# Performance work log

Measured on AMD Instinct MI355X. Metric: run time of the kernel, lower is better.

Reference implementation:

```python
import jax, jax.numpy as jnp
import numpy as np

WS = 8          # window_size
NH = 8          # num_heads
DIM = 512
EPS = 1e-5


def _layernorm(x, gamma, beta):
    mu = jnp.mean(x, axis=-1, keepdims=True)
    var = jnp.mean(jnp.square(x - mu), axis=-1, keepdims=True)
    return (x - mu) * jax.lax.rsqrt(var + EPS) * gamma + beta


def setup_inputs() -> dict:
    key = jax.random.key(0)
    ks = jax.random.split(key, 16)
    B, C, H, W = 8, DIM, 128, 128
    s = 0.02
    return {
        "x": jax.random.normal(ks[0], (B, C, H, W), jnp.float32),
        "gamma1": jnp.ones((C,), jnp.float32),
        "beta1": jnp.zeros((C,), jnp.float32),
        "gamma2": jnp.ones((C,), jnp.float32),
        "beta2": jnp.zeros((C,), jnp.float32),
        "w_qkv": jax.random.normal(ks[1], (C, 3 * C), jnp.float32) * s,
        "b_qkv": jnp.zeros((3 * C,), jnp.float32),
        "w_out": jax.random.normal(ks[2], (C, C), jnp.float32) * s,
        "b_out": jnp.zeros((C,), jnp.float32),
        "w1": jax.random.normal(ks[3], (C, 4 * C), jnp.float32) * s,
        "b1": jnp.zeros((4 * C,), jnp.float32),
        "w2": jax.random.normal(ks[4], (4 * C, C), jnp.float32) * s,
        "b2": jnp.zeros((C,), jnp.float32),
    }


def reference(x, gamma1, beta1, gamma2, beta2, w_qkv, b_qkv, w_out, b_out, w1, b1, w2, b2):
    B, C, H, W = x.shape
    hd = C // NH          # head_dim = 64
    L = WS * WS           # tokens per window = 64
    N = (H // WS) * (W // WS)

    # window_partition: (B,C,H,W) -> (B,N,C,ws,ws)
    xw = x.reshape(B, C, H // WS, WS, W // WS, WS)
    xw = xw.transpose(0, 1, 2, 4, 3, 5).reshape(B, C, N, WS, WS).transpose(0, 2, 1, 3, 4)
    # spatial_flatten -> (B,N,L,C)
    t = xw.reshape(B, N, C, L).transpose(0, 1, 3, 2)

    # --- attention (non-transposed path) ---
    xn = _layernorm(t, gamma1, beta1)
    qkv = jnp.einsum('bnlc,cd->bnld', xn, w_qkv) + b_qkv
    qkv = qkv.reshape(B, N, L, 3, NH, hd).transpose(3, 0, 1, 4, 2, 5)  # (3,B,N,H,L,hd)
    q, k, v = qkv[0], qkv[1], qkv[2]
    # note: module scales by 1/head_dim on BOTH q and k -> 1/hd^2 total
    scores = jnp.einsum('bnhld,bnhmd->bnhlm', q, k) / (hd * hd)
    attn = jax.nn.softmax(scores, axis=-1)
    o = jnp.einsum('bnhlm,bnhmd->bnhld', attn, v)
    o = o.transpose(0, 1, 3, 2, 4).reshape(B, N, L, C)
    o = jnp.einsum('bnlc,cd->bnld', o, w_out) + b_out
    t = t + o

    # --- MLP ---
    xn2 = _layernorm(t, gamma2, beta2)
    h = jax.nn.gelu(jnp.einsum('bnlc,cd->bnld', xn2, w1) + b1, approximate=False)
    t = t + jnp.einsum('bnld,dc->bnlc', h, w2) + b2

    # spatial_unflatten + window_unpartition -> (B,C,H,W)
    y = t.transpose(0, 1, 3, 2).reshape(B, N, C, WS, WS).transpose(0, 2, 1, 3, 4)
    y = y.reshape(B, C, H // WS, W // WS, WS, WS).transpose(0, 1, 2, 4, 3, 5).reshape(B, C, H, W)
    return y
```

## Files before the change

### kernel.cpp

```cpp
#include <hip/hip_runtime.h>
#include <cstdint>
#include <cstddef>


typedef unsigned short u16;
typedef unsigned int u32;
typedef __attribute__((ext_vector_type(4))) float f32x4;
typedef __attribute__((ext_vector_type(8))) short bf16x8;

#define DEVINL __device__ __forceinline__

DEVINL float bf2f(u16 u){ union { u32 i; float f; } v; v.i = ((u32)u) << 16; return v.f; }
DEVINL u16 f2bf(float f){
  union { float f; u32 i; } v; v.f = f;
  u32 u = v.i;
  u32 r = (u + 0x7fffu + ((u >> 16) & 1u)) >> 16;
  return (u16)r;
}

DEVINL void gload16(u16* lds, const void* g){
  __builtin_amdgcn_global_load_lds(
      (__attribute__((address_space(1))) u32*)(g),
      (__attribute__((address_space(3))) u32*)(lds), 16, 0, 0);
}

__global__ __launch_bounds__(256) void wt_kernel(const float* __restrict__ in,
                                                 u16* __restrict__ out, int K, int N)
{
  __shared__ float tile[64][65];
  int tiles_n = N >> 6;
  int tk = blockIdx.x / tiles_n, tn = blockIdx.x % tiles_n;
  int k0 = tk * 64, n0 = tn * 64;
  int lane = threadIdx.x & 63, wr = threadIdx.x >> 6;
#pragma unroll
  for (int i = 0; i < 16; i++){
    int r = wr * 16 + i;
    tile[r][lane] = in[(size_t)(k0 + r) * N + n0 + lane];
  }
  __syncthreads();
#pragma unroll
  for (int i = 0; i < 16; i++){
    int r = wr * 16 + i;
    out[(size_t)(n0 + r) * K + k0 + lane] = f2bf(tile[lane][r]);
  }
}

template<int MODE>
__global__ __launch_bounds__(256) void ln_kernel(
    const float* __restrict__ x, const u16* __restrict__ o2,
    const float* __restrict__ gamma, const float* __restrict__ beta,
    u16* __restrict__ out)
{
  __shared__ u16 sm[512 * 64];
  int wg = blockIdx.x;
  int b = wg >> 8, n = wg & 255, wy = n >> 4, wx = n & 15;
  int t = threadIdx.x, l = t & 63, wv = t >> 6;
  int yy = l >> 3, xx = l & 7;
  size_t xbase = ((size_t)b * 512) * 16384 + (size_t)(wy * 8 + yy) * 128 + wx * 8 + xx;

#pragma unroll 4
  for (int i = 0; i < 128; i++){
    int c = wv * 128 + i;
    float v = x[xbase + (size_t)c * 16384];
    sm[c * 64 + (l ^ ((2 * (c >> 3)) & 63))] = f2bf(v);
  }
  __syncthreads();

  size_t gbase = (size_t)wg * 64;
  int lane = l;
  int c0 = lane * 8;
  int fs = (2 * lane) & 63;
  float g8[8], b8[8];
#pragma unroll
  for (int j = 0; j < 8; j++){ g8[j] = gamma[c0 + j]; b8[j] = beta[c0 + j]; }

  for (int it = 0; it < 16; it++){
    int tok = wv * 16 + it;
    int lidx = tok ^ fs;
    u16 oarr[8];
    if (MODE == 1){
      uint4 ov = *(const uint4*)&o2[(gbase + tok) * 512 + c0];
      *(uint4*)oarr = ov;
    }
    float tv[8]; float sum = 0.f, sq = 0.f;
#pragma unroll
    for (int j = 0; j < 8; j++){
      float v = bf2f(sm[(c0 + j) * 64 + lidx]);
      if (MODE == 1) v += bf2f(oarr[j]);
      tv[j] = v; sum += v; sq += v * v;
    }
#pragma unroll
    for (int d = 1; d < 64; d <<= 1){
      sum += __shfl_xor(sum, d, 64);
      sq  += __shfl_xor(sq, d, 64);
    }
    float mu = sum * (1.0f / 512.0f);
    float var = sq * (1.0f / 512.0f) - mu * mu;
    float rs = rsqrtf(var + 1e-5f);
    u16 r8[8];
#pragma unroll
    for (int j = 0; j < 8; j++) r8[j] = f2bf((tv[j] - mu) * rs * g8[j] + b8[j]);
    *(uint4*)&out[(gbase + tok) * 512 + c0] = *(uint4*)r8;
  }
}

template<int EPI>
__global__ __launch_bounds__(512, 2) void gemm256_kernel(
    const u16* __restrict__ A, const u16* __restrict__ BT,
    const float* __restrict__ bias, const u16* __restrict__ ADD,
    u16* __restrict__ Cout, int N, int K)
{
  __shared__ u16 smem[65536];
  const int nbn = N >> 8;
  int nwg = gridDim.x;
  int bid = blockIdx.x;
  int wgid = (bid & 7) * (nwg >> 3) + (bid >> 3);
  int bm = wgid / nbn, bn = wgid % nbn;
  size_t m0 = (size_t)bm * 256; int n0 = bn * 256;
  int tid = threadIdx.x;
  int lane = tid & 63, w = tid >> 6;
  int wr = w >> 2, wc = w & 3;

  f32x4 zero4 = {0.f, 0.f, 0.f, 0.f};
  f32x4 acc[8][4];
#pragma unroll
  for (int i = 0; i < 8; i++)
#pragma unroll
    for (int j = 0; j < 4; j++) acc[i][j] = zero4;

  int sr = tid >> 2;
  int scol = (((tid & 3) ^ ((sr >> 1) & 3)) * 8);
  const u16* Abase = A + m0 * (size_t)K;
  const u16* Bbase = BT + (size_t)n0 * K;

  auto STAGE = [&](int slot, int kt){
    u16* s = &smem[slot * 16384];
    gload16(s + w * 512,          Abase + (size_t)sr * K + kt + scol);
    gload16(s + 4096 + w * 512,   Abase + (size_t)(sr + 128) * K + kt + scol);
    gload16(s + 8192 + w * 512,   Bbase + (size_t)sr * K + kt + scol);
    gload16(s + 12288 + w * 512,  Bbase + (size_t)(sr + 128) * K + kt + scol);
  };

  int nk = K >> 5;
  STAGE(0, 0); STAGE(1, 32); STAGE(2, 64);

  int kslot = lane >> 4;
  for (int t = 0; t < nk; ++t){
    if (t < nk - 2)      asm volatile("s_waitcnt vmcnt(8)" ::: "memory");
    else if (t == nk - 2) asm volatile("s_waitcnt vmcnt(4)" ::: "memory");
    else                  asm volatile("s_waitcnt vmcnt(0)" ::: "memory");
    __builtin_amdgcn_s_barrier();
    if (t + 3 < nk) STAGE((t + 3) & 3, (t + 3) << 5);

    const u16* as = &smem[(t & 3) * 16384];
    const u16* bs = as + 8192;
    bf16x8 af[8], bf[4];
#pragma unroll
    for (int m = 0; m < 8; m++){
      int row = wr * 128 + m * 16 + (lane & 15);
      af[m] = *(const bf16x8*)&as[row * 32 + ((kslot ^ ((row >> 1) & 3)) * 8)];
    }
#pragma unroll
    for (int n = 0; n < 4; n++){
      int row = wc * 64 + n * 16 + (lane & 15);
      bf[n] = *(const bf16x8*)&bs[row * 32 + ((kslot ^ ((row >> 1) & 3)) * 8)];
    }
    __builtin_amdgcn_s_setprio(1);
#pragma unroll
    for (int m = 0; m < 8; m++)
#pragma unroll
      for (int n = 0; n < 4; n++)
        acc[m][n] = __builtin_amdgcn_mfma_f32_16x16x32_bf16(af[m], bf[n], acc[m][n], 0, 0, 0);
    __builtin_amdgcn_s_setprio(0);
  }

  __syncthreads();

#pragma unroll
  for (int n = 0; n < 4; n++){
    int cc = wc * 64 + n * 16 + (lane & 15);
    float bv = bias[n0 + cc];
#pragma unroll
    for (int m = 0; m < 8; m++){
      int r0 = wr * 128 + m * 16 + ((lane >> 4) * 4);
#pragma unroll
      for (int reg = 0; reg < 4; reg++){
        int rr = r0 + reg;
        float v = acc[m][n][reg] + bv;
        if (EPI == 1){
          float h2 = v * v;
          float z = -1.5957691216057308f * (v + 0.044715f * v * h2);
          float e = __expf(z);
          v = v * __builtin_amdgcn_rcpf(1.0f + e);
        }
        smem[rr * 256 + (cc ^ ((rr & 31) << 3))] = f2bf(v);
      }
    }
  }
  __syncthreads();

#pragma unroll
  for (int i = 0; i < 16; i++){
    int c = i * 512 + tid;
    int row = c >> 5, g = c & 31;
    size_t gro = (m0 + row) * (size_t)N + n0 + g * 8;
    uint4 d = *(const uint4*)&smem[row * 256 + ((g ^ (row & 31)) << 3)];
    if (EPI == 2){
      uint4 av = *(const uint4*)&ADD[gro];
      u16 de[8], ae[8];
      *(uint4*)de = d; *(uint4*)ae = av;
#pragma unroll
      for (int k = 0; k < 8; k++) de[k] = f2bf(bf2f(de[k]) + bf2f(ae[k]));
      d = *(uint4*)de;
    }
    *(uint4*)&Cout[gro] = d;
  }
}

__global__ __launch_bounds__(64) void attn_kernel(const u16* __restrict__ QKV,
                                                  u16* __restrict__ O)
{
  __shared__ u16 qs[4096], ks2[4096], vs[4096], ps[4096];
  int blk = blockIdx.x;
  int wg = blk >> 3, h = blk & 7;
  size_t g0 = (size_t)wg * 64;
  int lane = threadIdx.x;
  int lr = lane >> 3, lch = lane & 7;

#pragma unroll
  for (int it = 0; it < 8; it++){
    int r = it * 8 + lr;
    int sc = lch ^ (r & 7);
    {
      uint4 d = *(const uint4*)&QKV[(g0 + r) * 1536 + h * 64 + lch * 8];
      *(uint4*)&qs[r * 64 + sc * 8] = d;
    }
    {
      uint4 d = *(const uint4*)&QKV[(g0 + r) * 1536 + 512 + h * 64 + lch * 8];
      *(uint4*)&ks2[r * 64 + sc * 8] = d;
    }
    {
      uint4 d = *(const uint4*)&QKV[(g0 + r) * 1536 + 1024 + h * 64 + lch * 8];
      u16 e[8]; *(uint4*)e = d;
      int m = r;
#pragma unroll
      for (int j = 0; j < 8; j++){
        int dd = lch * 8 + j;
        int off = dd * 64 + ((((m * 2) ^ ((dd & 7) << 4))) >> 1);
        vs[off] = e[j];
      }
    }
  }
  __syncthreads();

  f32x4 zero4 = {0.f, 0.f, 0.f, 0.f};
  f32x4 s[4][4];
#pragma unroll
  for (int i = 0; i < 4; i++)
#pragma unroll
    for (int j = 0; j < 4; j++) s[i][j] = zero4;

#pragma unroll
  for (int ks = 0; ks < 2; ks++){
    bf16x8 aq[4], bk[4];
#pragma unroll
    for (int mt = 0; mt < 4; mt++){
      int r = mt * 16 + (lane & 15);
      int cb = (ks * 64 + (lane >> 4) * 16) ^ ((r & 7) << 4);
      aq[mt] = *(const bf16x8*)&qs[r * 64 + (cb >> 1)];
    }
#pragma unroll
    for (int nt = 0; nt < 4; nt++){
      int r = nt * 16 + (lane & 15);
      int cb = (ks * 64 + (lane >> 4) * 16) ^ ((r & 7) << 4);
      bk[nt] = *(const bf16x8*)&ks2[r * 64 + (cb >> 1)];
    }
#pragma unroll
    for (int mt = 0; mt < 4; mt++)
#pragma unroll
      for (int nt = 0; nt < 4; nt++)
        s[mt][nt] = __builtin_amdgcn_mfma_f32_16x16x32_bf16(aq[mt], bk[nt], s[mt][nt], 0, 0, 0);
  }

  const float scl = 1.0f / 4096.0f;
#pragma unroll
  for (int mt = 0; mt < 4; mt++){
#pragma unroll
    for (int reg = 0; reg < 4; reg++){
      float mx = -1e30f;
#pragma unroll
      for (int nt = 0; nt < 4; nt++){
        float v = s[mt][nt][reg] * scl; s[mt][nt][reg] = v; mx = fmaxf(mx, v);
      }
#pragma unroll
      for (int d = 1; d < 16; d <<= 1) mx = fmaxf(mx, __shfl_xor(mx, d, 64));
      float sum = 0.f;
#pragma unroll
      for (int nt = 0; nt < 4; nt++){
        float e = __expf(s[mt][nt][reg] - mx); s[mt][nt][reg] = e; sum += e;
      }
#pragma unroll
      for (int d = 1; d < 16; d <<= 1) sum += __shfl_xor(sum, d, 64);
      float inv = 1.0f / sum;
#pragma unroll
      for (int nt = 0; nt < 4; nt++) s[mt][nt][reg] *= inv;
    }
  }

#pragma unroll
  for (int mt = 0; mt < 4; mt++)
#pragma unroll
    for (int reg = 0; reg < 4; reg++){
      int r = mt * 16 + ((lane >> 4) * 4) + reg;
#pragma unroll
      for (int nt = 0; nt < 4; nt++){
        int c = nt * 16 + (lane & 15);
        ps[r * 64 + ((((c * 2) ^ ((r & 7) << 4))) >> 1)] = f2bf(s[mt][nt][reg]);
      }
    }
  __syncthreads();

  f32x4 o[4][4];
#pragma unroll
  for (int i = 0; i < 4; i++)
#pragma unroll
    for (int j = 0; j < 4; j++) o[i][j] = zero4;

#pragma unroll
  for (int ks = 0; ks < 2; ks++){
    bf16x8 ap[4], bv[4];
#pragma unroll
    for (int mt = 0; mt < 4; mt++){
      int r = mt * 16 + (lane & 15);
      int cb = (ks * 64 + (lane >> 4) * 16) ^ ((r & 7) << 4);
      ap[mt] = *(const bf16x8*)&ps[r * 64 + (cb >> 1)];
    }
#pragma unroll
    for (int nt = 0; nt < 4; nt++){
      int dd = nt * 16 + (lane & 15);
      int cb = (ks * 64 + (lane >> 4) * 16) ^ ((dd & 7) << 4);
      bv[nt] = *(const bf16x8*)&vs[dd * 64 + (cb >> 1)];
    }
#pragma unroll
    for (int mt = 0; mt < 4; mt++)
#pragma unroll
      for (int nt = 0; nt < 4; nt++)
        o[mt][nt] = __builtin_amdgcn_mfma_f32_16x16x32_bf16(ap[mt], bv[nt], o[mt][nt], 0, 0, 0);
  }

#pragma unroll
  for (int mt = 0; mt < 4; mt++)
#pragma unroll
    for (int reg = 0; reg < 4; reg++){
      size_t l = mt * 16 + ((lane >> 4) * 4) + reg;
#pragma unroll
      for (int nt = 0; nt < 4; nt++){
        int dd = nt * 16 + (lane & 15);
        O[(g0 + l) * 512 + h * 64 + dd] = f2bf(o[mt][nt][reg]);
      }
    }
}

__global__ __launch_bounds__(256) void scatter_kernel(
    const float* __restrict__ x, const u16* __restrict__ ms, float* __restrict__ y)
{
  __shared__ u16 sm[512 * 64];
  int wg = blockIdx.x;
  int b = wg >> 8, n = wg & 255, wy = n >> 4, wx = n & 15;
  int t = threadIdx.x, lane = t & 63, wv = t >> 6;
  size_t gbase = (size_t)wg * 64;
  int c0 = lane * 8, fs = (2 * lane) & 63;

  for (int it = 0; it < 16; it++){
    int tok = wv * 16 + it;
    uint4 d = *(const uint4*)&ms[(gbase + tok) * 512 + c0];
    u16 e[8]; *(uint4*)e = d;
    int lidx = tok ^ fs;
#pragma unroll
    for (int j = 0; j < 8; j++) sm[(c0 + j) * 64 + lidx] = e[j];
  }
  __syncthreads();

  int l = lane; int yy = l >> 3, xx = l & 7;
  size_t xbase = ((size_t)b * 512) * 16384 + (size_t)(wy * 8 + yy) * 128 + wx * 8 + xx;
#pragma unroll 4
  for (int i = 0; i < 128; i++){
    int c = wv * 128 + i;
    size_t a = xbase + (size_t)c * 16384;
    y[a] = x[a] + bf2f(sm[c * 64 + (l ^ ((2 * (c >> 3)) & 63))]);
  }
}

extern "C" void kernel_launch(void* const* d_in, const int* in_sizes, int n_in,
                              void* d_out, int out_size, void* d_ws, size_t ws_size,
                              hipStream_t stream)
{
  (void)in_sizes; (void)n_in; (void)out_size; (void)ws_size;
  const float* x      = (const float*)d_in[0];
  const float* gamma1 = (const float*)d_in[1];
  const float* beta1  = (const float*)d_in[2];
  const float* gamma2 = (const float*)d_in[3];
  const float* beta2  = (const float*)d_in[4];
  const float* w_qkv  = (const float*)d_in[5];
  const float* b_qkv  = (const float*)d_in[6];
  const float* w_out  = (const float*)d_in[7];
  const float* b_out  = (const float*)d_in[8];
  const float* w1     = (const float*)d_in[9];
  const float* b1     = (const float*)d_in[10];
  const float* w2     = (const float*)d_in[11];
  const float* b2     = (const float*)d_in[12];
  float* y = (float*)d_out;

  char* ws = (char*)d_ws;
  u16* WqkvT = (u16*)(ws + 0);
  u16* WoutT = (u16*)(ws + 1572864);
  u16* W1T   = (u16*)(ws + 2097152);
  u16* W2T   = (u16*)(ws + 4194304);
  u16* XN    = (u16*)(ws + 6291456);
  u16* O2    = (u16*)(ws + 140509184);
  u16* Obuf  = (u16*)(ws + 274726912);
  u16* QKV   = (u16*)(ws + 408944640);
  u16* Hbuf  = QKV;
  u16* MS    = Obuf;
  const int M = 131072;

  wt_kernel<<<8 * 24, 256, 0, stream>>>(w_qkv, WqkvT, 512, 1536);
  wt_kernel<<<8 * 8,  256, 0, stream>>>(w_out, WoutT, 512, 512);
  wt_kernel<<<8 * 32, 256, 0, stream>>>(w1, W1T, 512, 2048);
  wt_kernel<<<32 * 8, 256, 0, stream>>>(w2, W2T, 2048, 512);

  ln_kernel<0><<<2048, 256, 0, stream>>>(x, nullptr, gamma1, beta1, XN);
  gemm256_kernel<0><<<(M / 256) * (1536 / 256), 512, 0, stream>>>(XN, WqkvT, b_qkv, nullptr, QKV, 1536, 512);
  attn_kernel<<<16384, 64, 0, stream>>>(QKV, Obuf);
  gemm256_kernel<0><<<(M / 256) * (512 / 256), 512, 0, stream>>>(Obuf, WoutT, b_out, nullptr, O2, 512, 512);
  ln_kernel<1><<<2048, 256, 0, stream>>>(x, O2, gamma2, beta2, XN);
  gemm256_kernel<1><<<(M / 256) * (2048 / 256), 512, 0, stream>>>(XN, W1T, b1, nullptr, Hbuf, 2048, 512);
  gemm256_kernel<2><<<(M / 256) * (512 / 256), 512, 0, stream>>>(Hbuf, W2T, b2, O2, MS, 512, 2048);
  scatter_kernel<<<2048, 256, 0, stream>>>(x, MS, y);
}
```

Measured before the change: 2.362 ms.

## Restructure GEMM main loop into ping-pong double buffer with interleaved load/MFMA phases

Replaces the 4-slot, K=32 staged pipeline in the 256x256 GEMM with a 2-buffer, K=64 scheme in which each iteration is split into four phases. Each phase issues LDS fragment reads for half the A rows, one async global-to-LDS load for the next tile, and a 16-MFMA block, separated by barriers. The goal is to interleave global loads, LDS reads and MFMA work more finely and to cut register pressure by holding only 4 A fragments at a time. In exchange it adds many more workgroup barriers per K step and reduces prefetch depth from three tiles ahead to one.

```diff
diff --git a/kernel.cpp b/kernel.cpp
--- a/kernel.cpp
+++ b/kernel.cpp
@@ -102,6 +102,22 @@
     for (int j = 0; j < 8; j++) r8[j] = f2bf((tv[j] - mu) * rs * g8[j] + b8[j]);
     *(uint4*)&out[(gbase + tok) * 512 + c0] = *(uint4*)r8;
   }
+}
+
+#define GBAR  __builtin_amdgcn_s_barrier()
+#define LGKM0 do { asm volatile("s_waitcnt lgkmcnt(0)" ::: "memory"); \
+                   __builtin_amdgcn_sched_barrier(0); } while(0)
+#define VM4   asm volatile("s_waitcnt vmcnt(4)" ::: "memory")
+#define VM0   asm volatile("s_waitcnt vmcnt(0)" ::: "memory")
+
+DEVINL void mfma_blk(f32x4 (&acc)[8][4], const bf16x8 (&ar)[4], const bf16x8 (&br)[4], int mh){
+  __builtin_amdgcn_s_setprio(1);
+#pragma unroll
+  for (int m = 0; m < 4; m++)
+#pragma unroll
+    for (int n = 0; n < 4; n++)
+      acc[mh * 4 + m][n] = __builtin_amdgcn_mfma_f32_16x16x32_bf16(ar[m], br[n], acc[mh * 4 + m][n], 0, 0, 0);
+  __builtin_amdgcn_s_setprio(0);
 }
 
 template<int EPI>
@@ -120,6 +136,7 @@
   int tid = threadIdx.x;
   int lane = tid & 63, w = tid >> 6;
   int wr = w >> 2, wc = w & 3;
+  int kslot = lane >> 4;
 
   f32x4 zero4 = {0.f, 0.f, 0.f, 0.f};
   f32x4 acc[8][4];
@@ -133,48 +150,64 @@
   const u16* Abase = A + m0 * (size_t)K;
   const u16* Bbase = BT + (size_t)n0 * K;
 
-  auto STAGE = [&](int slot, int kt){
-    u16* s = &smem[slot * 16384];
-    gload16(s + w * 512,          Abase + (size_t)sr * K + kt + scol);
-    gload16(s + 4096 + w * 512,   Abase + (size_t)(sr + 128) * K + kt + scol);
-    gload16(s + 8192 + w * 512,   Bbase + (size_t)sr * K + kt + scol);
-    gload16(s + 12288 + w * 512,  Bbase + (size_t)(sr + 128) * K + kt + scol);
+  auto SU = [&](int b16, const u16* src, int kcol){
+    gload16(&smem[b16] + w * 512,        src + (size_t)sr * K + kcol);
+    gload16(&smem[b16] + 4096 + w * 512, src + (size_t)(sr + 128) * K + kcol);
   };
 
-  int nk = K >> 5;
-  STAGE(0, 0); STAGE(1, 32); STAGE(2, 64);
-
-  int kslot = lane >> 4;
-  for (int t = 0; t < nk; ++t){
-    if (t < nk - 2)      asm volatile("s_waitcnt vmcnt(8)" ::: "memory");
-    else if (t == nk - 2) asm volatile("s_waitcnt vmcnt(4)" ::: "memory");
-    else                  asm volatile("s_waitcnt vmcnt(0)" ::: "memory");
-    __builtin_amdgcn_s_barrier();
-    if (t + 3 < nk) STAGE((t + 3) & 3, (t + 3) << 5);
-
-    const u16* as = &smem[(t & 3) * 16384];
-    const u16* bs = as + 8192;
-    bf16x8 af[8], bf[4];
-#pragma unroll
-    for (int m = 0; m < 8; m++){
-      int row = wr * 128 + m * 16 + (lane & 15);
-      af[m] = *(const bf16x8*)&as[row * 32 + ((kslot ^ ((row >> 1) & 3)) * 8)];
-    }
+  auto RDA = [&](bf16x8 (&ar)[4], int cb, int mh, int ks){
+#pragma unroll
+    for (int m = 0; m < 4; m++){
+      int row = wr * 128 + (mh * 4 + m) * 16 + (lane & 15);
+      ar[m] = *(const bf16x8*)&smem[cb + ks * 8192 + row * 32 + ((kslot ^ ((row >> 1) & 3)) * 8)];
+    }
+  };
+  auto RDB = [&](bf16x8 (&br)[4], int cb, int ks){
 #pragma unroll
     for (int n = 0; n < 4; n++){
       int row = wc * 64 + n * 16 + (lane & 15);
-      bf[n] = *(const bf16x8*)&bs[row * 32 + ((kslot ^ ((row >> 1) & 3)) * 8)];
-    }
-    __builtin_amdgcn_s_setprio(1);
-#pragma unroll
-    for (int m = 0; m < 8; m++)
-#pragma unroll
-      for (int n = 0; n < 4; n++)
-        acc[m][n] = __builtin_amdgcn_mfma_f32_16x16x32_bf16(af[m], bf[n], acc[m][n], 0, 0, 0);
-    __builtin_amdgcn_s_setprio(0);
-  }
-
-  __syncthreads();
+      br[n] = *(const bf16x8*)&smem[cb + 16384 + ks * 8192 + row * 32 + ((kslot ^ ((row >> 1) & 3)) * 8)];
+    }
+  };
+
+  SU(0,     Abase, scol);
+  SU(16384, Bbase, scol);
+  SU(8192,  Abase, 32 + scol);
+  SU(24576, Bbase, 32 + scol);
+  VM4;
+  GBAR;
+
+  int nk = K >> 6;
+  for (int t = 0; t < nk; ++t){
+    int cb = (t & 1) << 15;
+    int nb = ((t + 1) & 1) << 15;
+    int ktn = (t + 1) << 6;
+    bool st = (t + 1 < nk);
+    bf16x8 areg[4], breg[4];
+
+    RDB(breg, cb, 0);
+    RDA(areg, cb, 0, 0);
+    if (st) SU(nb, Abase, ktn + scol);
+    GBAR; LGKM0;
+    mfma_blk(acc, areg, breg, 0);
+    GBAR;
+    RDA(areg, cb, 1, 0);
+    if (st){ SU(nb + 16384, Bbase, ktn + scol); VM4; } else { VM0; }
+    GBAR; LGKM0;
+    mfma_blk(acc, areg, breg, 1);
+    GBAR;
+    RDB(breg, cb, 1);
+    RDA(areg, cb, 0, 1);
+    if (st) SU(nb + 8192, Abase, ktn + 32 + scol);
+    GBAR; LGKM0;
+    mfma_blk(acc, areg, breg, 0);
+    GBAR;
+    RDA(areg, cb, 1, 1);
+    if (st){ SU(nb + 24576, Bbase, ktn + 32 + scol); VM4; }
+    GBAR; LGKM0;
+    mfma_blk(acc, areg, breg, 1);
+    GBAR;
+  }
 
 #pragma unroll
   for (int n = 0; n < 4; n++){
```

New measurement: 2.349 ms. About the same (-0.5%).
